# Optimization experiments

Hardware: AMD Instinct MI355X
Metric: run time of the kernel (lower is better)

The kernel has to match this reference:

```python
import jax, jax.numpy as jnp
import numpy as np

HIDDEN = 512
HEADS = 8
HEAD_DIM = HIDDEN // HEADS


def setup_inputs() -> dict:
    key = jax.random.key(0)
    ks = jax.random.split(key, 9)
    B, S = 4, 2048
    scale = 1.0 / np.sqrt(HIDDEN)
    x = jax.random.normal(ks[0], (B, S, HIDDEN), dtype=jnp.float32)
    Wq = jax.random.normal(ks[1], (HIDDEN, HIDDEN), dtype=jnp.float32) * scale
    Wk = jax.random.normal(ks[2], (HIDDEN, HIDDEN), dtype=jnp.float32) * scale
    Wv = jax.random.normal(ks[3], (HIDDEN, HIDDEN), dtype=jnp.float32) * scale
    Wo = jax.random.normal(ks[4], (HIDDEN, HIDDEN), dtype=jnp.float32) * scale
    bq = jax.random.normal(ks[5], (HIDDEN,), dtype=jnp.float32) * 0.01
    bk = jax.random.normal(ks[6], (HIDDEN,), dtype=jnp.float32) * 0.01
    bv = jax.random.normal(ks[7], (HIDDEN,), dtype=jnp.float32) * 0.01
    bo = jax.random.normal(ks[8], (HIDDEN,), dtype=jnp.float32) * 0.01
    return {"x": x, "Wq": Wq, "bq": bq, "Wk": Wk, "bk": bk,
            "Wv": Wv, "bv": bv, "Wo": Wo, "bo": bo}


def reference(x, Wq, bq, Wk, bk, Wv, bv, Wo, bo):
    B, S, _ = x.shape
    # project and split heads: [B, H, S, D]
    def split_heads(t):
        return t.reshape(B, S, HEADS, HEAD_DIM).transpose(0, 2, 1, 3)
    Q = split_heads(x @ Wq.T + bq)
    K = split_heads(x @ Wk.T + bk)
    V = split_heads(x @ Wv.T + bv)
    scores = jnp.einsum("bhsd,bhtd->bhst", Q, K) / jnp.sqrt(
        jnp.array(HEAD_DIM, dtype=x.dtype))
    attn = jax.nn.softmax(scores, axis=-1)  # dropout is identity in eval
    ctx = jnp.einsum("bhst,bhtd->bhsd", attn, V)
    ctx = ctx.transpose(0, 2, 1, 3).reshape(B, S, HIDDEN)
    return ctx @ Wo.T + bo
```

## Files before the change

kernel.cpp:

```cpp
#include <hip/hip_runtime.h>
#include <stdint.h>

#define HID 512
#define NH 8
#define HD 64
#define BB 4
#define SS 2048

typedef unsigned short u16;
typedef __attribute__((ext_vector_type(8))) short short8;
typedef __attribute__((ext_vector_type(4))) float f32x4;
typedef __attribute__((ext_vector_type(4))) _Float16 f16x4;
typedef __attribute__((ext_vector_type(2))) unsigned int uint2v;

#define MFMA16(a, b, c) __builtin_amdgcn_mfma_f32_16x16x32_bf16((a), (b), (c), 0, 0, 0)
#define MFMAH16(a, b, c) __builtin_amdgcn_mfma_f32_16x16x16f16((a), (b), (c), 0, 0, 0)

#define WAIT_VM8() __builtin_amdgcn_s_waitcnt(0xF78)
#define WAIT_VM4() __builtin_amdgcn_s_waitcnt(0xF74)
#define WAIT_VM3() __builtin_amdgcn_s_waitcnt(0xF73)
#define WAIT_VM0() __builtin_amdgcn_s_waitcnt(0xF70)
#define PIPE_BARRIER() do { asm volatile("" ::: "memory"); \
  __builtin_amdgcn_s_barrier(); asm volatile("" ::: "memory"); } while (0)

__device__ __forceinline__ u16 f2bf(float f) {
  union { float f; uint32_t u; } v; v.f = f;
  return (u16)((v.u + 0x7fffu + ((v.u >> 16) & 1u)) >> 16);
}

__device__ __forceinline__ u16 f2h(float f) {
  _Float16 h = (_Float16)f;
  return __builtin_bit_cast(u16, h);
}

__device__ __forceinline__ void gl_lds16(const u16* g, u16* l) {
  __builtin_amdgcn_global_load_lds(
      (const __attribute__((address_space(1))) unsigned int*)g,
      (__attribute__((address_space(3))) unsigned int*)l, 16, 0, 0);
}

__global__ void prep(const float* __restrict__ x,
                     const float* __restrict__ w0, const float* __restrict__ w1,
                     const float* __restrict__ w2, const float* __restrict__ w3,
                     u16* __restrict__ xb,
                     u16* __restrict__ o0, u16* __restrict__ o1,
                     u16* __restrict__ o2, u16* __restrict__ o3) {
  const int bid = blockIdx.x;
  const float* in;
  u16* out;
  int base;
  if (bid < 4096) {
    in = x; out = xb; base = bid * 1024;
  } else {
    const int z = (bid - 4096) >> 8;
    base = ((bid - 4096) & 255) * 1024;
    in = (z == 0) ? w0 : (z == 1) ? w1 : (z == 2) ? w2 : w3;
    out = (z == 0) ? o0 : (z == 1) ? o1 : (z == 2) ? o2 : o3;
  }
  const int i = base + threadIdx.x * 4;
  float4 v = *(const float4*)(in + i);
  ushort4 o;
  o.x = f2bf(v.x); o.y = f2bf(v.y); o.z = f2bf(v.z); o.w = f2bf(v.w);
  *(ushort4*)(out + i) = o;
}

__global__ __launch_bounds__(256, 3)
void qkv_gemm(const u16* __restrict__ xb,
              const u16* __restrict__ wq, const u16* __restrict__ wk, const u16* __restrict__ wv,
              const float* __restrict__ bq, const float* __restrict__ bk, const float* __restrict__ bv,
              u16* __restrict__ Q, u16* __restrict__ K, u16* __restrict__ Vt) {
  __shared__ u16 sA[3][4096];
  __shared__ u16 sB[3][4096];
  const int tid = threadIdx.x;
  const int lane = tid & 63;
  const int wave = tid >> 6;
  const int l15 = lane & 15;
  const int quad = lane >> 4;
  const int wm = wave >> 1, wn = wave & 1;

  const int L = blockIdx.x;
  const int xcd = L & 7;
  const int slot = L >> 3;
  const int bm = xcd * 8 + (slot & 7);
  const int r2 = slot >> 3;
  const int bn = r2 & 3;
  const int z = r2 >> 2;

  const float* bias = (z == 0) ? bq : (z == 1) ? bk : bv;
  const float scale = (z == 0) ? 0.18033688011112042f : 1.0f;

  const u16* Arows = (z == 2) ? wv : xb;
  const u16* Brows = (z == 2) ? xb : ((z == 0) ? wq : wk);
  const int am0 = (z == 2) ? (bn * 128) : (bm * 128);
  const int bn0 = (z == 2) ? (bm * 128) : (bn * 128);

  const int srow = tid >> 2;
  const int sg = (tid & 3) ^ ((srow >> 1) & 3);
  const u16* gA = Arows + (am0 + srow) * 512 + sg * 8;
  const u16* gB = Brows + (bn0 + srow) * 512 + sg * 8;

  const int fsw = (quad ^ ((l15 >> 1) & 3)) * 8;
  int aoff[4], boff[4];
#pragma unroll
  for (int t = 0; t < 4; ++t) {
    aoff[t] = (wm * 64 + t * 16 + l15) * 32 + fsw;
    boff[t] = (wn * 64 + t * 16 + l15) * 32 + fsw;
  }

  f32x4 acc[4][4] = {};

#pragma unroll
  for (int t = 0; t < 2; ++t) {
    const int k0 = t * 32;
    gl_lds16(gA + k0, &sA[t][wave * 512]);
    gl_lds16(gA + k0 + 64 * 512, &sA[t][2048 + wave * 512]);
    gl_lds16(gB + k0, &sB[t][wave * 512]);
    gl_lds16(gB + k0 + 64 * 512, &sB[t][2048 + wave * 512]);
  }

  for (int kk = 0; kk < 16; ++kk) {
    WAIT_VM4();
    PIPE_BARRIER();
    {
      const int tp = (kk + 2 < 16) ? kk + 2 : 15;
      const int ns = (kk + 2) % 3;
      const int k0 = tp * 32;
      gl_lds16(gA + k0, &sA[ns][wave * 512]);
      gl_lds16(gA + k0 + 64 * 512, &sA[ns][2048 + wave * 512]);
      gl_lds16(gB + k0, &sB[ns][wave * 512]);
      gl_lds16(gB + k0 + 64 * 512, &sB[ns][2048 + wave * 512]);
    }
    const int cur = kk % 3;
    short8 af[4], bf[4];
#pragma unroll
    for (int t = 0; t < 4; ++t) af[t] = *(const short8*)&sA[cur][aoff[t]];
#pragma unroll
    for (int t = 0; t < 4; ++t) bf[t] = *(const short8*)&sB[cur][boff[t]];
#pragma unroll
    for (int mi = 0; mi < 4; ++mi)
#pragma unroll
      for (int ni = 0; ni < 4; ++ni)
        acc[mi][ni] = MFMA16(af[mi], bf[ni], acc[mi][ni]);
  }

  if (z != 2) {
    u16* dst = (z == 0) ? Q : K;
#pragma unroll
    for (int mi = 0; mi < 4; ++mi) {
#pragma unroll
      for (int ni = 0; ni < 4; ++ni) {
        const int col = bn0 + wn * 64 + ni * 16 + l15;
        const float bs = bias[col];
#pragma unroll
        for (int i = 0; i < 4; ++i) {
          const int row = am0 + wm * 64 + mi * 16 + quad * 4 + i;
          const float v = (acc[mi][ni][i] + bs) * scale;
          const int b = row >> 11, s = row & 2047;
          const int h = col >> 6, d = col & 63;
          dst[(((size_t)(b * 8 + h) * 2048 + s) << 6) + d] = f2bf(v);
        }
      }
    }
  } else {
#pragma unroll
    for (int mi = 0; mi < 4; ++mi) {
#pragma unroll
      for (int i = 0; i < 4; ++i) {
        const int o = am0 + wm * 64 + mi * 16 + quad * 4 + i;
        const float bs = bias[o];
        const int h = o >> 6, d = o & 63;
#pragma unroll
        for (int ni = 0; ni < 4; ++ni) {
          const int r = bn0 + wn * 64 + ni * 16 + l15;
          const int b = r >> 11, s = r & 2047;
          Vt[(((size_t)(b * 8 + h) * 64 + d) << 11) + s] = f2h(acc[mi][ni][i] + bs);
        }
      }
    }
  }
}

__global__ __launch_bounds__(256, 2)
void attn(const u16* __restrict__ Q, const u16* __restrict__ K,
          const u16* __restrict__ Vt, u16* __restrict__ ctx) {
  __shared__ __align__(16) u16 smem[4 * 8192];
  const int tid = threadIdx.x;
  const int lane = tid & 63;
  const int wave = tid >> 6;
  const int l15 = lane & 15;
  const int quad = lane >> 4;
  const int pair = wave >> 1;
  const int par = wave & 1;

  const int L = blockIdx.x;
  const int xcd = L & 7;
  const int slotb = L >> 3;
  const int bh = xcd * 4 + (slotb & 3);
  const int qt = slotb >> 2;

  const u16* Qb = Q + (size_t)bh * SS * HD;
  const u16* Kb = K + (size_t)bh * SS * HD;
  const u16* Vb = Vt + (size_t)bh * HD * SS;

  const int rowbase = qt * 128 + pair * 64;
  short8 qf[4][2];
#pragma unroll
  for (int rf = 0; rf < 4; ++rf)
#pragma unroll
    for (int kc = 0; kc < 2; ++kc)
      qf[rf][kc] = *(const short8*)(Qb + (rowbase + rf * 16 + l15) * 64 + kc * 32 + quad * 8);
  asm volatile("" ::: "memory");

  f32x4 oacc[4][4] = {};
  float plsum[4] = {0.f, 0.f, 0.f, 0.f};

  const int trow = tid >> 3;
  const int gsw = (tid & 7) ^ (trow & 7);
  const int kOff = trow * 64 + gsw * 8;
  const int vOff = trow * 2048 + gsw * 8;
  u16* ldsK = smem + tid * 8;
  u16* ldsV = smem + 4096 + tid * 8;

  const int l7 = l15 & 7;
  int kfo[2];
#pragma unroll
  for (int kc = 0; kc < 2; ++kc)
    kfo[kc] = (par * 32 + l15) * 64 + ((kc * 4 + quad) ^ l7) * 8;
  int vfo[2];
#pragma unroll
  for (int tb = 0; tb < 2; ++tb)
    vfo[tb] = l15 * 64 + (((par * 4 + tb * 2 + (quad >> 1)) ^ l7) * 8) + (quad & 1) * 4;

#pragma unroll
  for (int t = 0; t < 3; ++t) {
    gl_lds16(Kb + t * 4096 + kOff, ldsK + t * 8192);
    gl_lds16(Kb + t * 4096 + kOff + 32 * 64, ldsK + t * 8192 + 2048);
    gl_lds16(Vb + t * 64 + vOff, ldsV + t * 8192);
    gl_lds16(Vb + t * 64 + vOff + 32 * 2048, ldsV + t * 8192 + 2048);
  }

  for (int tt = 0; tt < 32; ++tt) {
    WAIT_VM8();
    PIPE_BARRIER();
    {
      const int tp = (tt + 3 < 32) ? tt + 3 : 31;
      const int ns = (tt + 3) & 3;
      gl_lds16(Kb + tp * 4096 + kOff, ldsK + ns * 8192);
      gl_lds16(Kb + tp * 4096 + kOff + 32 * 64, ldsK + ns * 8192 + 2048);
      gl_lds16(Vb + tp * 64 + vOff, ldsV + ns * 8192);
      gl_lds16(Vb + tp * 64 + vOff + 32 * 2048, ldsV + ns * 8192 + 2048);
    }
    const int cb = (tt & 3) * 8192;

#pragma unroll
    for (int tb = 0; tb < 2; ++tb) {
      const short8 k0 = *(const short8*)&smem[cb + tb * 1024 + kfo[0]];
      const short8 k1 = *(const short8*)&smem[cb + tb * 1024 + kfo[1]];
      f32x4 sacc[4] = {};
#pragma unroll
      for (int rf = 0; rf < 4; ++rf) {
        sacc[rf] = MFMA16(k0, qf[rf][0], sacc[rf]);
        sacc[rf] = MFMA16(k1, qf[rf][1], sacc[rf]);
      }
      uint2v vf[4];
#pragma unroll
      for (int nd = 0; nd < 4; ++nd)
        vf[nd] = *(const uint2v*)&smem[cb + 4096 + nd * 1024 + vfo[tb]];
#pragma unroll
      for (int rf = 0; rf < 4; ++rf) {
        const float p0 = __builtin_amdgcn_exp2f(sacc[rf][0]);
        const float p1 = __builtin_amdgcn_exp2f(sacc[rf][1]);
        const float p2 = __builtin_amdgcn_exp2f(sacc[rf][2]);
        const float p3 = __builtin_amdgcn_exp2f(sacc[rf][3]);
        plsum[rf] += (p0 + p1) + (p2 + p3);
        uint2v pu;
        pu.x = __builtin_bit_cast(unsigned int, __builtin_amdgcn_cvt_pkrtz(p0, p1));
        pu.y = __builtin_bit_cast(unsigned int, __builtin_amdgcn_cvt_pkrtz(p2, p3));
        const f16x4 pf = __builtin_bit_cast(f16x4, pu);
#pragma unroll
        for (int nd = 0; nd < 4; ++nd)
          oacc[rf][nd] = MFMAH16(pf, __builtin_bit_cast(f16x4, vf[nd]), oacc[rf][nd]);
      }
    }
  }

  WAIT_VM0();
  __syncthreads();

#pragma unroll
  for (int rf = 0; rf < 4; ++rf) {
    plsum[rf] += __shfl_xor(plsum[rf], 16);
    plsum[rf] += __shfl_xor(plsum[rf], 32);
  }

  float* cbuf = (float*)smem;
  float* lbuf = cbuf + 128 * 68;
  if (par) {
#pragma unroll
    for (int rf = 0; rf < 4; ++rf) {
#pragma unroll
      for (int nd = 0; nd < 4; ++nd)
#pragma unroll
        for (int i = 0; i < 4; ++i)
          cbuf[(pair * 64 + rf * 16 + quad * 4 + i) * 68 + nd * 16 + l15] = oacc[rf][nd][i];
      if (quad == 0) lbuf[pair * 64 + rf * 16 + l15] = plsum[rf];
    }
  }
  __syncthreads();
  if (!par) {
    const int b = bh >> 3, h = bh & 7;
#pragma unroll
    for (int rf = 0; rf < 4; ++rf) {
      const float tot = plsum[rf] + lbuf[pair * 64 + rf * 16 + l15];
      float inv[4];
#pragma unroll
      for (int i = 0; i < 4; ++i)
        inv[i] = __builtin_amdgcn_rcpf(__shfl(tot, quad * 4 + i));
#pragma unroll
      for (int nd = 0; nd < 4; ++nd)
#pragma unroll
        for (int i = 0; i < 4; ++i) {
          const float v = (oacc[rf][nd][i] +
                           cbuf[(pair * 64 + rf * 16 + quad * 4 + i) * 68 + nd * 16 + l15]) * inv[i];
          const int s = rowbase + rf * 16 + quad * 4 + i;
          const int d = nd * 16 + l15;
          ctx[((size_t)(b * 2048 + s) << 9) + h * 64 + d] = f2bf(v);
        }
    }
  }
}

__global__ __launch_bounds__(256, 2)
void out_gemm(const u16* __restrict__ A, const u16* __restrict__ W,
              const float* __restrict__ bias, float* __restrict__ out) {
  __shared__ u16 sA[3][4096];
  __shared__ u16 sB[3][2048];
  const int tid = threadIdx.x;
  const int lane = tid & 63;
  const int wave = tid >> 6;
  const int l15 = lane & 15;
  const int quad = lane >> 4;

  const int L = blockIdx.x;
  const int xcd = L & 7;
  const int slot = L >> 3;
  const int bm = xcd * 8 + (slot & 7);
  const int bn = slot >> 3;

  const int srow = tid >> 2;
  const int sg = (tid & 3) ^ ((srow >> 1) & 3);
  const u16* gA = A + (bm * 128 + srow) * 512 + sg * 8;
  const u16* gB = W + (bn * 64 + srow) * 512 + sg * 8;

  const int fsw = (quad ^ ((l15 >> 1) & 3)) * 8;
  int aoff[2], boff[4];
#pragma unroll
  for (int t = 0; t < 2; ++t) aoff[t] = (wave * 32 + t * 16 + l15) * 32 + fsw;
#pragma unroll
  for (int t = 0; t < 4; ++t) boff[t] = (t * 16 + l15) * 32 + fsw;

  f32x4 acc[2][4] = {};

#pragma unroll
  for (int t = 0; t < 2; ++t) {
    const int k0 = t * 32;
    gl_lds16(gA + k0, &sA[t][wave * 512]);
    gl_lds16(gA + k0 + 64 * 512, &sA[t][2048 + wave * 512]);
    gl_lds16(gB + k0, &sB[t][wave * 512]);
  }

  for (int kk = 0; kk < 16; ++kk) {
    WAIT_VM3();
    PIPE_BARRIER();
    {
      const int tp = (kk + 2 < 16) ? kk + 2 : 15;
      const int ns = (kk + 2) % 3;
      const int k0 = tp * 32;
      gl_lds16(gA + k0, &sA[ns][wave * 512]);
      gl_lds16(gA + k0 + 64 * 512, &sA[ns][2048 + wave * 512]);
      gl_lds16(gB + k0, &sB[ns][wave * 512]);
    }
    const int cur = kk % 3;
    short8 af[2], bf[4];
#pragma unroll
    for (int t = 0; t < 2; ++t) af[t] = *(const short8*)&sA[cur][aoff[t]];
#pragma unroll
    for (int t = 0; t < 4; ++t) bf[t] = *(const short8*)&sB[cur][boff[t]];
#pragma unroll
    for (int mi = 0; mi < 2; ++mi)
#pragma unroll
      for (int ni = 0; ni < 4; ++ni)
        acc[mi][ni] = MFMA16(af[mi], bf[ni], acc[mi][ni]);
  }

#pragma unroll
  for (int mi = 0; mi < 2; ++mi) {
#pragma unroll
    for (int ni = 0; ni < 4; ++ni) {
      const int col = bn * 64 + ni * 16 + l15;
      const float bs = bias[col];
#pragma unroll
      for (int i = 0; i < 4; ++i) {
        const int row = bm * 128 + wave * 32 + mi * 16 + quad * 4 + i;
        out[(size_t)row * 512 + col] = acc[mi][ni][i] + bs;
      }
    }
  }
}

extern "C" void kernel_launch(void* const* d_in, const int* in_sizes, int n_in,
                              void* d_out, int out_size, void* d_ws, size_t ws_size,
                              hipStream_t stream) {
  const float* x = (const float*)d_in[0];
  const float* Wq = (const float*)d_in[1];
  const float* bq = (const float*)d_in[2];
  const float* Wk = (const float*)d_in[3];
  const float* bk = (const float*)d_in[4];
  const float* Wv = (const float*)d_in[5];
  const float* bv = (const float*)d_in[6];
  const float* Wo = (const float*)d_in[7];
  const float* bo = (const float*)d_in[8];
  float* out = (float*)d_out;

  char* ws = (char*)d_ws;
  u16* xb  = (u16*)(ws);
  u16* wqb = (u16*)(ws + (8u << 20));
  u16* wkb = (u16*)(ws + (8u << 20) + (512u << 10));
  u16* wvb = (u16*)(ws + (9u << 20));
  u16* wob = (u16*)(ws + (9u << 20) + (512u << 10));
  u16* Qb  = (u16*)(ws + (10u << 20));
  u16* Kb  = (u16*)(ws + (18u << 20));
  u16* Vtb = (u16*)(ws + (26u << 20));
  u16* ctx = (u16*)(ws + (34u << 20));

  prep<<<5120, 256, 0, stream>>>(x, Wq, Wk, Wv, Wo, xb, wqb, wkb, wvb, wob);
  qkv_gemm<<<768, 256, 0, stream>>>(xb, wqb, wkb, wvb, bq, bk, bv, Qb, Kb, Vtb);
  attn<<<512, 256, 0, stream>>>(Qb, Kb, Vtb, ctx);
  out_gemm<<<512, 256, 0, stream>>>(ctx, wob, bo, out);
}
```

Measured before the change: 157.3 us.

## Split attention KV loop across four waves per row group with 512-thread blocks

The attention kernel now runs 512 threads per block, with four waves (instead of two) sharing each 64-row query group, each handling a quarter of every KV tile. The KV pipeline changes from a 4-stage single-tile ring to double buffering of two tiles per iteration, with a full vmcnt(0) wait before each barrier. The epilogue becomes a tree reduction of partial output accumulators and row sums through LDS over several barriers. The aim is more waves per CU to hide latency. The cost is shallower prefetch, more sync points and a longer reduction.

```diff
diff --git a/kernel.cpp b/kernel.cpp
--- a/kernel.cpp
+++ b/kernel.cpp
@@ -16,7 +16,6 @@
 #define MFMA16(a, b, c) __builtin_amdgcn_mfma_f32_16x16x32_bf16((a), (b), (c), 0, 0, 0)
 #define MFMAH16(a, b, c) __builtin_amdgcn_mfma_f32_16x16x16f16((a), (b), (c), 0, 0, 0)
 
-#define WAIT_VM8() __builtin_amdgcn_s_waitcnt(0xF78)
 #define WAIT_VM4() __builtin_amdgcn_s_waitcnt(0xF74)
 #define WAIT_VM3() __builtin_amdgcn_s_waitcnt(0xF73)
 #define WAIT_VM0() __builtin_amdgcn_s_waitcnt(0xF70)
@@ -180,17 +179,17 @@
   }
 }
 
-__global__ __launch_bounds__(256, 2)
+__global__ __launch_bounds__(512, 4)
 void attn(const u16* __restrict__ Q, const u16* __restrict__ K,
           const u16* __restrict__ Vt, u16* __restrict__ ctx) {
-  __shared__ __align__(16) u16 smem[4 * 8192];
+  __shared__ __align__(16) u16 smem[2 * 16384];
   const int tid = threadIdx.x;
   const int lane = tid & 63;
   const int wave = tid >> 6;
   const int l15 = lane & 15;
   const int quad = lane >> 4;
-  const int pair = wave >> 1;
-  const int par = wave & 1;
+  const int pair = wave >> 2;
+  const int par = wave & 3;
 
   const int L = blockIdx.x;
   const int xcd = L & 7;
@@ -216,46 +215,41 @@
 
   const int trow = tid >> 3;
   const int gsw = (tid & 7) ^ (trow & 7);
-  const int kOff = trow * 64 + gsw * 8;
-  const int vOff = trow * 2048 + gsw * 8;
-  u16* ldsK = smem + tid * 8;
-  u16* ldsV = smem + 4096 + tid * 8;
+  const u16* gK = Kb + trow * 64 + gsw * 8;
+  const u16* gV = Vb + trow * 2048 + gsw * 8;
+  u16* lK = smem + tid * 8;
+  u16* lV = smem + 4096 + tid * 8;
 
   const int l7 = l15 & 7;
   int kfo[2];
 #pragma unroll
   for (int kc = 0; kc < 2; ++kc)
-    kfo[kc] = (par * 32 + l15) * 64 + ((kc * 4 + quad) ^ l7) * 8;
-  int vfo[2];
-#pragma unroll
-  for (int tb = 0; tb < 2; ++tb)
-    vfo[tb] = l15 * 64 + (((par * 4 + tb * 2 + (quad >> 1)) ^ l7) * 8) + (quad & 1) * 4;
-
-#pragma unroll
-  for (int t = 0; t < 3; ++t) {
-    gl_lds16(Kb + t * 4096 + kOff, ldsK + t * 8192);
-    gl_lds16(Kb + t * 4096 + kOff + 32 * 64, ldsK + t * 8192 + 2048);
-    gl_lds16(Vb + t * 64 + vOff, ldsV + t * 8192);
-    gl_lds16(Vb + t * 64 + vOff + 32 * 2048, ldsV + t * 8192 + 2048);
-  }
-
-  for (int tt = 0; tt < 32; ++tt) {
-    WAIT_VM8();
+    kfo[kc] = (par * 16 + l15) * 64 + ((kc * 4 + quad) ^ l7) * 8;
+  const int vfo = l15 * 64 + (((par * 2 + (quad >> 1)) ^ l7) * 8) + (quad & 1) * 4;
+
+#pragma unroll
+  for (int tp = 0; tp < 2; ++tp) {
+    gl_lds16(gK + tp * 4096, lK + tp * 8192);
+    gl_lds16(gV + tp * 64, lV + tp * 8192);
+  }
+
+  for (int u = 0; u < 16; ++u) {
+    WAIT_VM0();
     PIPE_BARRIER();
-    {
-      const int tp = (tt + 3 < 32) ? tt + 3 : 31;
-      const int ns = (tt + 3) & 3;
-      gl_lds16(Kb + tp * 4096 + kOff, ldsK + ns * 8192);
-      gl_lds16(Kb + tp * 4096 + kOff + 32 * 64, ldsK + ns * 8192 + 2048);
-      gl_lds16(Vb + tp * 64 + vOff, ldsV + ns * 8192);
-      gl_lds16(Vb + tp * 64 + vOff + 32 * 2048, ldsV + ns * 8192 + 2048);
-    }
-    const int cb = (tt & 3) * 8192;
-
-#pragma unroll
-    for (int tb = 0; tb < 2; ++tb) {
-      const short8 k0 = *(const short8*)&smem[cb + tb * 1024 + kfo[0]];
-      const short8 k1 = *(const short8*)&smem[cb + tb * 1024 + kfo[1]];
+    if (u + 1 < 16) {
+      const int ns = (u + 1) & 1;
+#pragma unroll
+      for (int tp = 0; tp < 2; ++tp) {
+        const int T = (u + 1) * 2 + tp;
+        gl_lds16(gK + T * 4096, lK + ns * 16384 + tp * 8192);
+        gl_lds16(gV + T * 64, lV + ns * 16384 + tp * 8192);
+      }
+    }
+#pragma unroll
+    for (int tp = 0; tp < 2; ++tp) {
+      const int cb = (u & 1) * 16384 + tp * 8192;
+      const short8 k0 = *(const short8*)&smem[cb + kfo[0]];
+      const short8 k1 = *(const short8*)&smem[cb + kfo[1]];
       f32x4 sacc[4] = {};
 #pragma unroll
       for (int rf = 0; rf < 4; ++rf) {
@@ -265,7 +259,7 @@
       uint2v vf[4];
 #pragma unroll
       for (int nd = 0; nd < 4; ++nd)
-        vf[nd] = *(const uint2v*)&smem[cb + 4096 + nd * 1024 + vfo[tb]];
+        vf[nd] = *(const uint2v*)&smem[cb + 4096 + nd * 1024 + vfo];
 #pragma unroll
       for (int rf = 0; rf < 4; ++rf) {
         const float p0 = __builtin_amdgcn_exp2f(sacc[rf][0]);
@@ -284,7 +278,6 @@
     }
   }
 
-  WAIT_VM0();
   __syncthreads();
 
 #pragma unroll
@@ -293,35 +286,73 @@
     plsum[rf] += __shfl_xor(plsum[rf], 32);
   }
 
-  float* cbuf = (float*)smem;
-  float* lbuf = cbuf + 128 * 68;
-  if (par) {
+  float* fb = (float*)smem;
+  const int rbase = pair * 64;
+
+  if (par != 0 && quad == 0) {
+#pragma unroll
+    for (int rf = 0; rf < 4; ++rf)
+      fb[(par - 1) * 128 + rbase + rf * 16 + l15] = plsum[rf];
+  }
+  __syncthreads();
+  float tot[4];
+  if (par == 0) {
 #pragma unroll
     for (int rf = 0; rf < 4; ++rf) {
+      const int r = rbase + rf * 16 + l15;
+      tot[rf] = plsum[rf] + fb[r] + fb[128 + r] + fb[256 + r];
+    }
+  }
+  __syncthreads();
+
+  if (par & 1) {
+    float* base = fb + (pair * 2 + (par >> 1)) * 4096;
+#pragma unroll
+    for (int rf = 0; rf < 4; ++rf)
 #pragma unroll
       for (int nd = 0; nd < 4; ++nd)
 #pragma unroll
         for (int i = 0; i < 4; ++i)
-          cbuf[(pair * 64 + rf * 16 + quad * 4 + i) * 68 + nd * 16 + l15] = oacc[rf][nd][i];
-      if (quad == 0) lbuf[pair * 64 + rf * 16 + l15] = plsum[rf];
-    }
-  }
-  __syncthreads();
-  if (!par) {
+          base[(rf * 16 + quad * 4 + i) * 64 + ((nd ^ quad) * 16 + l15)] = oacc[rf][nd][i];
+  }
+  __syncthreads();
+  if (!(par & 1)) {
+    const float* base = fb + (pair * 2 + (par >> 1)) * 4096;
+#pragma unroll
+    for (int rf = 0; rf < 4; ++rf)
+#pragma unroll
+      for (int nd = 0; nd < 4; ++nd)
+#pragma unroll
+        for (int i = 0; i < 4; ++i)
+          oacc[rf][nd][i] += base[(rf * 16 + quad * 4 + i) * 64 + ((nd ^ quad) * 16 + l15)];
+  }
+  __syncthreads();
+  if (par == 2) {
+    float* base = fb + pair * 4096;
+#pragma unroll
+    for (int rf = 0; rf < 4; ++rf)
+#pragma unroll
+      for (int nd = 0; nd < 4; ++nd)
+#pragma unroll
+        for (int i = 0; i < 4; ++i)
+          base[(rf * 16 + quad * 4 + i) * 64 + ((nd ^ quad) * 16 + l15)] = oacc[rf][nd][i];
+  }
+  __syncthreads();
+  if (par == 0) {
+    const float* base = fb + pair * 4096;
     const int b = bh >> 3, h = bh & 7;
 #pragma unroll
     for (int rf = 0; rf < 4; ++rf) {
-      const float tot = plsum[rf] + lbuf[pair * 64 + rf * 16 + l15];
       float inv[4];
 #pragma unroll
       for (int i = 0; i < 4; ++i)
-        inv[i] = __builtin_amdgcn_rcpf(__shfl(tot, quad * 4 + i));
+        inv[i] = __builtin_amdgcn_rcpf(__shfl(tot[rf], quad * 4 + i));
 #pragma unroll
       for (int nd = 0; nd < 4; ++nd)
 #pragma unroll
         for (int i = 0; i < 4; ++i) {
           const float v = (oacc[rf][nd][i] +
-                           cbuf[(pair * 64 + rf * 16 + quad * 4 + i) * 68 + nd * 16 + l15]) * inv[i];
+                           base[(rf * 16 + quad * 4 + i) * 64 + ((nd ^ quad) * 16 + l15)]) * inv[i];
           const int s = rowbase + rf * 16 + quad * 4 + i;
           const int d = nd * 16 + l15;
           ctx[((size_t)(b * 2048 + s) << 9) + h * 64 + d] = f2bf(v);
@@ -435,6 +466,6 @@
 
   prep<<<5120, 256, 0, stream>>>(x, Wq, Wk, Wv, Wo, xb, wqb, wkb, wvb, wob);
   qkv_gemm<<<768, 256, 0, stream>>>(xb, wqb, wkb, wvb, bq, bk, bv, Qb, Kb, Vtb);
-  attn<<<512, 256, 0, stream>>>(Qb, Kb, Vtb, ctx);
+  attn<<<512, 512, 0, stream>>>(Qb, Kb, Vtb, ctx);
   out_gemm<<<512, 256, 0, stream>>>(ctx, wob, bo, out);
 }
```

New measurement: 284.7 us. 1.81x slower.
